# Kernel tuning notes

Hardware: AMD Instinct MI355X
Metric: run time of the kernel (lower is better)

Reference implementation:

```python
import jax, jax.numpy as jnp
import numpy as np

N = 50000        # nodes
E = 1_600_000    # edges (before self-loops)
H = 2            # heads
C = 16           # out channels per head
G = 512          # graphs in batch
F_IN = 3         # const + degree + rand
NC = 2           # classes
NEG_SLOPE = 0.2  # PyG GATv2Conv default


def setup_inputs() -> dict:
    key = jax.random.key(0)
    ks = jax.random.split(key, 12)
    p = lambda k, shape: (jax.random.normal(k, shape, dtype=jnp.float32) * 0.1)
    edge_index = jax.random.randint(ks[0], (2, E), 0, N, dtype=jnp.int64)
    batch = jnp.sort(jax.random.randint(ks[1], (N,), 0, G, dtype=jnp.int64))
    rand_feat = jax.random.uniform(ks[2], (N, 1), dtype=jnp.float32)
    return {
        "edge_index": edge_index,
        "batch": batch,
        "rand_feat": rand_feat,
        # conv1: in=3 -> H*C=32
        "W1l": p(ks[3], (H * C, F_IN)), "b1l": jnp.zeros((H * C,), jnp.float32),
        "W1r": p(ks[4], (H * C, F_IN)), "b1r": jnp.zeros((H * C,), jnp.float32),
        "att1": p(ks[5], (H, C)), "bias1": jnp.zeros((H * C,), jnp.float32),
        # conv2: in=32 -> 32
        "W2l": p(ks[6], (H * C, H * C)), "b2l": jnp.zeros((H * C,), jnp.float32),
        "W2r": p(ks[7], (H * C, H * C)), "b2r": jnp.zeros((H * C,), jnp.float32),
        "att2": p(ks[8], (H, C)), "bias2": jnp.zeros((H * C,), jnp.float32),
        # fc: 32 -> 2
        "Wfc": p(ks[9], (NC, H * C)), "bfc": jnp.zeros((NC,), jnp.float32),
    }


def gatv2_conv(x, src, dst, Wl, bl, Wr, br, att, bias):
    """PyG GATv2Conv (concat=True, self-loops already appended to src/dst)."""
    n = x.shape[0]
    xl = (x @ Wl.T + bl).reshape(n, H, C)   # messages / values
    xr = (x @ Wr.T + br).reshape(n, H, C)   # target-side term
    m = xl[src] + xr[dst]                   # [E', H, C]
    e = jnp.where(m > 0, m, NEG_SLOPE * m)  # LeakyReLU
    score = jnp.einsum('ehc,hc->eh', e, att)
    # segment softmax over destination nodes (every node has a self-loop)
    smax = jax.ops.segment_max(score, dst, num_segments=n)
    ex = jnp.exp(score - smax[dst])
    denom = jax.ops.segment_sum(ex, dst, num_segments=n)
    alpha = ex / (denom[dst] + 1e-16)
    out = jax.ops.segment_sum(xl[src] * alpha[:, :, None], dst, num_segments=n)
    return out.reshape(n, H * C) + bias


def reference(edge_index, batch, rand_feat, W1l, b1l, W1r, b1r, att1, bias1,
              W2l, b2l, W2r, b2r, att2, bias2, Wfc, bfc):
    src, dst = edge_index[0], edge_index[1]
    # degree feature: index_add of ones over both rows (original edges only)
    ones_e = jnp.ones((E,), jnp.float32)
    deg = (jax.ops.segment_sum(ones_e, src, num_segments=N)
           + jax.ops.segment_sum(ones_e, dst, num_segments=N))
    x = jnp.concatenate([jnp.ones((N, 1), jnp.float32), deg[:, None], rand_feat], axis=1)
    # PyG GATv2Conv adds self-loops by default
    loops = jnp.arange(N, dtype=src.dtype)
    src_sl = jnp.concatenate([src, loops])
    dst_sl = jnp.concatenate([dst, loops])
    x = jax.nn.elu(gatv2_conv(x, src_sl, dst_sl, W1l, b1l, W1r, b1r, att1, bias1))
    x = jax.nn.elu(gatv2_conv(x, src_sl, dst_sl, W2l, b2l, W2r, b2r, att2, bias2))
    # global mean pool over graphs
    sums = jax.ops.segment_sum(x, batch, num_segments=G)
    counts = jax.ops.segment_sum(jnp.ones((N,), jnp.float32), batch, num_segments=G)
    pooled = sums / jnp.clip(counts, 1.0)[:, None]
    logits = pooled @ Wfc.T + bfc
    return jax.nn.log_softmax(logits, axis=1)
```

## Files before the change

kernel.cpp:

```cpp
#include <hip/hip_runtime.h>
#include <hip/hip_fp16.h>
#include <math.h>

#define HC 32
#define CH 16
#define NSLOPE 0.2f
#define NB2MAX 512
#define TILE 8192
#define CBMAX 6144
#define NSL 128
#define HGRP 8
#define HLDS 12544

__device__ __forceinline__ unsigned gen_pair(const int* __restrict__ ei, int E, int i){
    if (i < E) return (unsigned(ei[E+i]) << 16) | unsigned(ei[i]);
    unsigned n = i - E; return (n << 16) | n;
}

__device__ __forceinline__ __half2 pkmax2(__half2 a, __half2 b){
    union { __half2 h; unsigned u; } ua, ub, ud;
    ua.h = a; ub.h = b;
    asm("v_pk_max_f16 %0, %1, %2" : "=v"(ud.u) : "v"(ua.u), "v"(ub.u));
    return ud.h;
}

__device__ __forceinline__ __half2 sfx2(__half2 x, int off){
    union { __half2 h; int i; } u; u.h = x;
    u.i = __shfl_xor(u.i, off);
    return u.h;
}

__global__ void k_hsrc(const int* __restrict__ ei, int E, int halfN,
                       unsigned* __restrict__ hb, unsigned* __restrict__ gPair){
    __shared__ unsigned h[HLDS];
    __shared__ unsigned hp[NB2MAX];
    int t = threadIdx.x;
    int nWloc = halfN >> 1;
    for (int i = t; i < nWloc; i += 512) h[i] = 0;
    int p = blockIdx.x & 1;
    if (p == 0){ hp[t] = 0; }
    __syncthreads();
    int slice = blockIdx.x >> 1;
    int base  = p * halfN;
    int chunk = (((E + NSL - 1) / NSL) + 3) & ~3;
    int lo = slice*chunk, hi = lo + chunk; if (hi > E) hi = E;
    bool v4 = ((E & 3) == 0);
    if (v4 && lo < hi){
        int m4 = lo + ((hi - lo) & ~3);
        for (int i = lo + 4*t; i + 3 < hi; i += 4*512){
            int4 s4 = *(const int4*)(ei + i);
            int a0 = s4.x - base, a1 = s4.y - base, a2 = s4.z - base, a3 = s4.w - base;
            if ((unsigned)a0 < (unsigned)halfN) atomicAdd(&h[a0 >> 1], 1u << (16*(a0 & 1)));
            if ((unsigned)a1 < (unsigned)halfN) atomicAdd(&h[a1 >> 1], 1u << (16*(a1 & 1)));
            if ((unsigned)a2 < (unsigned)halfN) atomicAdd(&h[a2 >> 1], 1u << (16*(a2 & 1)));
            if ((unsigned)a3 < (unsigned)halfN) atomicAdd(&h[a3 >> 1], 1u << (16*(a3 & 1)));
            if (p == 0){
                int4 d4 = *(const int4*)(ei + E + i);
                atomicAdd(&hp[unsigned(d4.x) >> 7], 1u);
                atomicAdd(&hp[unsigned(d4.y) >> 7], 1u);
                atomicAdd(&hp[unsigned(d4.z) >> 7], 1u);
                atomicAdd(&hp[unsigned(d4.w) >> 7], 1u);
            }
        }
        for (int i = m4 + t; i < hi; i += 512){
            int s = ei[i] - base;
            if ((unsigned)s < (unsigned)halfN) atomicAdd(&h[s >> 1], 1u << (16*(s & 1)));
            if (p == 0) atomicAdd(&hp[unsigned(ei[E+i]) >> 7], 1u);
        }
    } else {
        for (int i = lo + t; i < hi; i += 512){
            int s = ei[i] - base;
            if ((unsigned)s < (unsigned)halfN) atomicAdd(&h[s >> 1], 1u << (16*(s & 1)));
            if (p == 0) atomicAdd(&hp[unsigned(ei[E+i]) >> 7], 1u);
        }
    }
    __syncthreads();
    unsigned* out = hb + (size_t)blockIdx.x * nWloc;
    for (int w = t; w < nWloc; w += 512) out[w] = h[w];
    if (p == 0 && hp[t]) atomicAdd(&gPair[t], hp[t]);
}

__global__ void k_hred(const unsigned* __restrict__ hb, unsigned* __restrict__ degS,
                       int nWloc,
                       const int* __restrict__ batch, int* __restrict__ gb,
                       int N, int G){
    int idx = blockIdx.x*blockDim.x + threadIdx.x;
    if (idx <= G){
        int lo = 0, hi = N;
        while (lo < hi){ int mid = (lo+hi)>>1; if (batch[mid] < idx) lo = mid+1; else hi = mid; }
        gb[idx] = lo;
    }
    int total = 2*nWloc;
    int grp = idx / total;
    if (grp >= HGRP) return;
    int rem = idx - grp*total;
    int p = (rem < nWloc) ? 0 : 1;
    int w = rem - p*nWloc;
    unsigned s = 0;
    int sl0 = grp*(NSL/HGRP), sl1 = sl0 + NSL/HGRP;
    for (int sl = sl0; sl < sl1; ++sl)
        s += hb[(size_t)(sl*2 + p)*nWloc + w];
    if (s) atomicAdd(&degS[rem], s);
}

__global__ void k_setup(unsigned* __restrict__ gPair,
                        int* __restrict__ partBase, int* __restrict__ gcur,
                        int* __restrict__ rsN, int EP, int nb, int N,
                        const float* __restrict__ W1l, const float* __restrict__ b1l,
                        const float* __restrict__ W1r, const float* __restrict__ b1r,
                        const float* __restrict__ att1, const float* __restrict__ bias1,
                        float4* __restrict__ tabA, float4* __restrict__ tabB){
    __shared__ int sp[NB2MAX];
    int t = threadIdx.x;
    int vp = 0;
    if (t < nb){
        int selfc = N - t*128;
        selfc = (selfc < 0) ? 0 : (selfc > 128 ? 128 : selfc);
        vp = (int)gPair[t] + selfc;
        gPair[t] = (unsigned)vp;
    }
    sp[t] = vp;
    __syncthreads();
    for (int d = 1; d < NB2MAX; d <<= 1){
        int x = (t >= d) ? sp[t-d] : 0;
        __syncthreads();
        sp[t] += x;
        __syncthreads();
    }
    if (t < nb){ partBase[t] = sp[t] - vp; gcur[t] = sp[t] - vp; }
    if (t == 0) rsN[0] = EP;
    if (t < HC){
        tabA[t] = make_float4(W1l[t*3] + b1l[t], W1l[t*3+1], W1l[t*3+2], att1[t]);
        tabB[t] = make_float4(W1r[t*3] + b1r[t], W1r[t*3+1], W1r[t*3+2], bias1[t]);
    }
}

__global__ void k_p2(const int* __restrict__ ei, int E, int EP,
                     int* __restrict__ gcur, unsigned* __restrict__ part){
    __shared__ int bcnt[NB2MAX], bstart[NB2MAX], c2[NB2MAX], gpos[NB2MAX], sc[256];
    __shared__ unsigned sorted[TILE];
    __shared__ unsigned short bktof[TILE];
    int t = threadIdx.x;
    int base = blockIdx.x * TILE;
    int cnt = EP - base; if (cnt > TILE) cnt = TILE;
    bool full = (cnt == TILE);

    bcnt[t] = 0; bcnt[t+256] = 0; c2[t] = 0; c2[t+256] = 0;
    __syncthreads();
    unsigned ec[TILE/256];
    if (full){
        #pragma unroll
        for (int q = 0; q < TILE/256; ++q)
            ec[q] = gen_pair(ei, E, base + t + q*256);
        #pragma unroll
        for (int q = 0; q < TILE/256; ++q)
            atomicAdd(&bcnt[ec[q] >> 23], 1);
    } else {
        for (int j = t; j < cnt; j += 256){
            unsigned e = gen_pair(ei, E, base + j);
            atomicAdd(&bcnt[e >> 23], 1);
        }
    }
    __syncthreads();
    int v0 = bcnt[2*t], v1 = bcnt[2*t+1];
    int s = v0 + v1;
    sc[t] = s;
    __syncthreads();
    for (int d = 1; d < 256; d <<= 1){
        int x = (t >= d) ? sc[t-d] : 0;
        __syncthreads();
        sc[t] += x;
        __syncthreads();
    }
    int excl = sc[t] - s;
    bstart[2*t]   = excl;
    bstart[2*t+1] = excl + v0;
    #pragma unroll
    for (int q = 0; q < 2; ++q){
        int bb = 2*t + q;
        int v = (q == 0) ? v0 : v1;
        if (v > 0){
            gpos[bb] = atomicAdd(&gcur[bb], v);
            int bs = bstart[bb];
            for (int j = 0; j < v; ++j) bktof[bs + j] = (unsigned short)bb;
        }
    }
    __syncthreads();
    if (full){
        #pragma unroll
        for (int q = 0; q < TILE/256; ++q){
            unsigned e = ec[q];
            int b = e >> 23;
            int off = atomicAdd(&c2[b], 1);
            sorted[bstart[b] + off] = e;
        }
    } else {
        for (int j = t; j < cnt; j += 256){
            unsigned e = gen_pair(ei, E, base + j);
            int b = e >> 23;
            int off = atomicAdd(&c2[b], 1);
            sorted[bstart[b] + off] = e;
        }
    }
    __syncthreads();
    for (int k = t; k < cnt; k += 256){
        int b = bktof[k];
        part[gpos[b] + (k - bstart[b])] = sorted[k];
    }
}

__global__ void k_fine(const unsigned* __restrict__ part, const int* __restrict__ partBase,
                       const unsigned* __restrict__ gPair,
                       const unsigned* __restrict__ degS, const float* __restrict__ rnd,
                       int* __restrict__ rs, float2* __restrict__ dr,
                       int* __restrict__ col, int N){
    __shared__ int pcnt[128], c2[128], lrs[129], sc[128];
    __shared__ int colbuf[CBMAX];
    int b = blockIdx.x, t = threadIdx.x;
    int beg = partBase[b], end = beg + (int)gPair[b];
    if (t < 128){ pcnt[t] = 0; c2[t] = 0; }
    __syncthreads();
    for (int k = beg + t; k < end; k += 256)
        atomicAdd(&pcnt[(part[k] >> 16) & 127], 1);
    __syncthreads();
    int v = (t < 128) ? pcnt[t] : 0;
    if (t < 128) sc[t] = v;
    __syncthreads();
    for (int d = 1; d < 128; d <<= 1){
        int x = (t >= d && t < 128) ? sc[t-d] : 0;
        __syncthreads();
        if (t < 128) sc[t] += x;
        __syncthreads();
    }
    if (t < 128){
        lrs[t] = sc[t] - v;
        if (t == 127) lrs[128] = sc[127];
    }
    __syncthreads();
    int n = (b << 7) + t;
    if (t < 128 && n < N){
        rs[n] = partBase[b] + lrs[t];
        unsigned s16 = (degS[n >> 1] >> (16*(n & 1))) & 0xFFFFu;
        dr[n] = make_float2((float)(pcnt[t] - 1 + (int)s16), rnd[n]);
    }
    for (int k = beg + t; k < end; k += 256){
        unsigned e = part[k];
        int j = (e >> 16) & 127;
        int pos = lrs[j] + atomicAdd(&c2[j], 1);
        if (pos < CBMAX) colbuf[pos] = (int)(e & 0xFFFFu);
    }
    __syncthreads();
    int npair = lrs[128];
    int cb = partBase[b];
    for (int k = t; k < npair; k += 256) col[cb + k] = colbuf[k];
}

__global__ void k_gat1(const int* __restrict__ rs, const int* __restrict__ col,
                       const float2* __restrict__ dr,
                       const float4* __restrict__ tabA, const float4* __restrict__ tabB,
                       const float* __restrict__ W2l, const float* __restrict__ b2l,
                       const float* __restrict__ W2r, const float* __restrict__ b2r,
                       __half* __restrict__ A16, __half* __restrict__ B16, int N){
    __shared__ float4 tA[HC], tB[HC];
    __shared__ float4 wq[HC][16];
    __shared__ float blS[HC], brS[HC];
    int t = threadIdx.x;
    if (t < HC){ tA[t] = tabA[t]; tB[t] = tabB[t]; blS[t] = b2l[t]; brS[t] = b2r[t]; }
    for (int w = t; w < HC*16; w += 256){
        int j = w >> 4, k = w & 15;
        wq[j][k] = make_float4(W2l[(2*k)*HC + j], W2l[(2*k+1)*HC + j],
                               W2r[(2*k)*HC + j], W2r[(2*k+1)*HC + j]);
    }
    __syncthreads();

    int d = blockIdx.x*(blockDim.x >> 4) + (t >> 4);
    if (d >= N) return;
    int lane = t & 15;
    int h = lane >> 3, r = lane & 7;

    float2 drd = dr[d];
    float base[CH];
    #pragma unroll
    for (int c = 0; c < CH; ++c){
        float4 a4 = tA[h*CH + c];
        float4 b4 = tB[h*CH + c];
        float xr = b4.x + b4.y*drd.x + b4.z*drd.y;
        base[c] = a4.x + xr;
    }

    float l = 0.f, S1 = 0.f, S2 = 0.f;
    int beg = rs[d], end = rs[d+1];
    int p = beg + r;
    for (; p + 8 < end; p += 16){
        int s0 = __builtin_nontemporal_load(col + p);
        int s1 = __builtin_nontemporal_load(col + p + 8);
        float2 da = dr[s0];
        float2 db = dr[s1];
        float sc0 = 0.f, sc1 = 0.f;
        #pragma unroll
        for (int c = 0; c < CH; ++c){
            float4 a4 = tA[h*CH + c];
            float m0 = base[c] + a4.y*da.x + a4.z*da.y;
            float m1 = base[c] + a4.y*db.x + a4.z*db.y;
            m0 = (m0 > 0.f) ? m0 : NSLOPE*m0;
            m1 = (m1 > 0.f) ? m1 : NSLOPE*m1;
            sc0 += m0 * a4.w;
            sc1 += m1 * a4.w;
        }
        float ex0 = __expf(sc0), ex1 = __expf(sc1);
        l  += ex0 + ex1;
        S1 += ex0*da.x + ex1*db.x;
        S2 += ex0*da.y + ex1*db.y;
    }
    if (p < end){
        float2 ds = dr[__builtin_nontemporal_load(col + p)];
        float sc = 0.f;
        #pragma unroll
        for (int c = 0; c < CH; ++c){
            float4 a4 = tA[h*CH + c];
            float mm = base[c] + a4.y*ds.x + a4.z*ds.y;
            mm = (mm > 0.f) ? mm : NSLOPE*mm;
            sc += mm * a4.w;
        }
        float ex = __expf(sc);
        l  += ex;
        S1 += ex*ds.x;
        S2 += ex*ds.y;
    }

    #pragma unroll
    for (int off = 4; off >= 1; off >>= 1){
        l  += __shfl_xor(l,  off);
        S1 += __shfl_xor(S1, off);
        S2 += __shfl_xor(S2, off);
    }

    float invl = 1.f/(l + 1e-16f);
    int c0 = r*2;
    float4 a40 = tA[h*CH + c0],     b40 = tB[h*CH + c0];
    float4 a41 = tA[h*CH + c0 + 1], b41 = tB[h*CH + c0 + 1];
    float v0 = a40.x + (a40.y*S1 + a40.z*S2)*invl + b40.w;
    float v1 = a41.x + (a41.y*S1 + a41.z*S2)*invl + b41.w;
    float x0 = (v0 > 0.f) ? v0 : expm1f(v0);
    float x1 = (v1 > 0.f) ? v1 : expm1f(v1);

    int k0 = 2*lane;
    float a0 = blS[k0], a1 = blS[k0+1];
    float g0 = brS[k0], g1 = brS[k0+1];
    #pragma unroll
    for (int tt = 0; tt < 16; ++tt){
        float xa = __shfl(x0, tt, 16);
        float xb = __shfl(x1, tt, 16);
        int j = 2*tt;
        float4 q0 = wq[j][lane];
        float4 q1 = wq[j+1][lane];
        a0 += xa*q0.x + xb*q1.x;
        a1 += xa*q0.y + xb*q1.y;
        g0 += xa*q0.z + xb*q1.z;
        g1 += xa*q0.w + xb*q1.w;
    }
    *(__half2*)(A16 + (size_t)d*HC + k0) = __floats2half2_rn(a0, a1);
    *(__half2*)(B16 + (size_t)d*HC + k0) = __floats2half2_rn(g0, g1);
}

__global__ void k_gat(const int* __restrict__ rs, const int* __restrict__ col,
                      const __half* __restrict__ A16, const __half* __restrict__ B16,
                      const float* __restrict__ att, const float* __restrict__ bias,
                      const int* __restrict__ batch, float* __restrict__ pooled, int N){
    __shared__ float pool[8][HC];
    __shared__ int sb[8];
    int sg = threadIdx.x >> 5;
    int d = blockIdx.x*(blockDim.x >> 5) + sg;
    int lane = threadIdx.x & 31;
    bool valid = (d < N);
    int dcl = valid ? d : 0;
    int h = lane >> 4, r = lane & 15;

    union U { uint4 u[2]; __half2 h2[8]; };
    U xr;
    {
        const uint4* bp = (const uint4*)(B16 + (size_t)dcl*HC + h*CH);
        xr.u[0] = bp[0]; xr.u[1] = bp[1];
    }
    __half2 at2[8];
    const float* atf = att + h*CH;
    #pragma unroll
    for (int i = 0; i < 8; ++i) at2[i] = __floats2half2_rn(atf[2*i], atf[2*i+1]);
    const __half2 ns2 = __float2half2_rn(NSLOPE);

    float l = 0.f;
    __half2 acc2[8];
    #pragma unroll
    for (int i = 0; i < 8; ++i) acc2[i] = __float2half2_rn(0.f);

    int beg = rs[dcl], end = valid ? rs[dcl+1] : beg;
    int p = beg + r;
    for (; p + 16 < end; p += 32){
        int s0 = __builtin_nontemporal_load(col + p);
        int s1 = __builtin_nontemporal_load(col + p + 16);
        const uint4* rp0 = (const uint4*)(A16 + (size_t)s0*HC + h*CH);
        const uint4* rp1 = (const uint4*)(A16 + (size_t)s1*HC + h*CH);
        U a, b;
        a.u[0] = rp0[0]; a.u[1] = rp0[1];
        b.u[0] = rp1[0]; b.u[1] = rp1[1];
        __half2 sc2 = __float2half2_rn(0.f);
        #pragma unroll
        for (int i = 0; i < 8; ++i){
            __half2 m  = __hadd2(a.h2[i], xr.h2[i]);
            __half2 lk = pkmax2(m, __hmul2(m, ns2));
            sc2 = __hfma2(lk, at2[i], sc2);
        }
        float ex = __expf(__low2float(sc2) + __high2float(sc2));
        l += ex;
        __half2 exh = __float2half2_rn(ex);
        #pragma unroll
        for (int i = 0; i < 8; ++i) acc2[i] = __hfma2(a.h2[i], exh, acc2[i]);

        sc2 = __float2half2_rn(0.f);
        #pragma unroll
        for (int i = 0; i < 8; ++i){
            __half2 m  = __hadd2(b.h2[i], xr.h2[i]);
            __half2 lk = pkmax2(m, __hmul2(m, ns2));
            sc2 = __hfma2(lk, at2[i], sc2);
        }
        ex = __expf(__low2float(sc2) + __high2float(sc2));
        l += ex;
        exh = __float2half2_rn(ex);
        #pragma unroll
        for (int i = 0; i < 8; ++i) acc2[i] = __hfma2(b.h2[i], exh, acc2[i]);
    }
    if (p < end){
        int s = __builtin_nontemporal_load(col + p);
        const uint4* rp = (const uint4*)(A16 + (size_t)s*HC + h*CH);
        U a;
        a.u[0] = rp[0]; a.u[1] = rp[1];
        __half2 sc2 = __float2half2_rn(0.f);
        #pragma unroll
        for (int i = 0; i < 8; ++i){
            __half2 m  = __hadd2(a.h2[i], xr.h2[i]);
            __half2 lk = pkmax2(m, __hmul2(m, ns2));
            sc2 = __hfma2(lk, at2[i], sc2);
        }
        float ex = __expf(__low2float(sc2) + __high2float(sc2));
        l += ex;
        __half2 exh = __float2half2_rn(ex);
        #pragma unroll
        for (int i = 0; i < 8; ++i) acc2[i] = __hfma2(a.h2[i], exh, acc2[i]);
    }

    __half2 v4[4];
    {
        bool hi = (r & 8) != 0;
        #pragma unroll
        for (int i = 0; i < 4; ++i){
            __half2 send = hi ? acc2[i] : acc2[i+4];
            __half2 recv = sfx2(send, 8);
            v4[i] = __hadd2(hi ? acc2[i+4] : acc2[i], recv);
        }
    }
    __half2 v2[2];
    {
        bool hi = (r & 4) != 0;
        __half2 s0 = hi ? v4[0] : v4[2];
        __half2 s1 = hi ? v4[1] : v4[3];
        __half2 r0 = sfx2(s0, 4);
        __half2 r1 = sfx2(s1, 4);
        v2[0] = __hadd2(hi ? v4[2] : v4[0], r0);
        v2[1] = __hadd2(hi ? v4[3] : v4[1], r1);
    }
    __half2 v1;
    {
        bool hi = (r & 2) != 0;
        __half2 send = hi ? v2[0] : v2[1];
        __half2 recv = sfx2(send, 2);
        v1 = __hadd2(hi ? v2[1] : v2[0], recv);
    }
    float mine;
    {
        bool hi = (r & 1) != 0;
        float lo = __low2float(v1), hf = __high2float(v1);
        float send = hi ? lo : hf;
        float recv = __shfl_xor(send, 1);
        mine = (hi ? hf : lo) + recv;
    }
    #pragma unroll
    for (int off = 8; off >= 1; off >>= 1) l += __shfl_xor(l, off);

    float invl = 1.f/(l + 1e-16f);
    float val = mine*invl + bias[h*CH + r];
    val = (val > 0.f) ? val : expm1f(val);

    if (lane == 0) sb[sg] = valid ? batch[d] : (-1 - sg);
    pool[sg][h*CH + r] = val;
    __syncthreads();
    int myb = sb[sg];
    int first = sg;
    #pragma unroll
    for (int j = 7; j >= 0; --j) if (sb[j] == myb) first = j;
    if (valid && first == sg){
        float s = 0.f;
        #pragma unroll
        for (int j = 0; j < 8; ++j) if (sb[j] == myb) s += pool[j][h*CH + r];
        atomicAdd(&pooled[(size_t)myb*HC + h*CH + r], s);
    }
}

__global__ void k_fc(const float* __restrict__ pooled, const int* __restrict__ gb,
                     const float* __restrict__ Wfc, const float* __restrict__ bfc,
                     float* __restrict__ out, int G){
    int t = threadIdx.x;
    int g = blockIdx.x*2 + (t >> 5);
    int c = t & 31;
    if (g >= G) return;
    float cnt = (float)(gb[g+1] - gb[g]);
    if (cnt < 1.f) cnt = 1.f;
    float pv = pooled[g*HC + c] / cnt;
    float p0 = pv * Wfc[c];
    float p1 = pv * Wfc[HC + c];
    #pragma unroll
    for (int off = 16; off >= 1; off >>= 1){
        p0 += __shfl_xor(p0, off, 32);
        p1 += __shfl_xor(p1, off, 32);
    }
    if (c == 0){
        float l0 = p0 + bfc[0], l1 = p1 + bfc[1];
        float m = (l0 > l1) ? l0 : l1;
        float lse = m + logf(__expf(l0 - m) + __expf(l1 - m));
        out[g*2 + 0] = l0 - lse;
        out[g*2 + 1] = l1 - lse;
    }
}

extern "C" void kernel_launch(void* const* d_in, const int* in_sizes, int n_in,
                              void* d_out, int out_size, void* d_ws, size_t ws_size,
                              hipStream_t stream) {
    const int*   ei    = (const int*)  d_in[0];
    const int*   batch = (const int*)  d_in[1];
    const float* rnd   = (const float*)d_in[2];
    const float* W1l   = (const float*)d_in[3];
    const float* b1l   = (const float*)d_in[4];
    const float* W1r   = (const float*)d_in[5];
    const float* b1r   = (const float*)d_in[6];
    const float* att1  = (const float*)d_in[7];
    const float* bias1 = (const float*)d_in[8];
    const float* W2l   = (const float*)d_in[9];
    const float* b2l   = (const float*)d_in[10];
    const float* W2r   = (const float*)d_in[11];
    const float* b2r   = (const float*)d_in[12];
    const float* att2  = (const float*)d_in[13];
    const float* bias2 = (const float*)d_in[14];
    const float* Wfc   = (const float*)d_in[15];
    const float* bfc   = (const float*)d_in[16];

    const int E  = in_sizes[0] / 2;
    const int N  = in_sizes[1];
    const int G  = out_size / 2;
    const int EP = E + N;
    const int NB2 = (N + 127) >> 7;
    const int halfN = (((N + 1) >> 1) + 1) & ~1;
    const int nWloc = halfN >> 1;

    float* ws        = (float*)d_ws;
    __half* A16      = (__half*)ws;
    __half* B16      = A16 + (size_t)N*HC;
    unsigned* hb     = (unsigned*)ws;
    unsigned* part   = (unsigned*)ws;
    size_t off       = (size_t)NSL*2*nWloc;
    if (off < (size_t)EP)   off = EP;
    if (off < (size_t)N*HC) off = (size_t)N*HC;
    off = (off + 1) & ~(size_t)1;
    float2* dr       = (float2*)(ws + off);
    int*   rs        = (int*)(dr + N);
    int*   col       = rs + N + 1;
    unsigned* degS   = (unsigned*)(col + EP);
    unsigned* gPair  = degS + 2*nWloc;
    float* pooled    = (float*)(gPair + NB2MAX);
    int*   partBase  = (int*)(pooled + (size_t)G*HC);
    int*   gcur      = partBase + NB2MAX;
    int*   gb        = gcur + NB2MAX;
    float4* tabA     = (float4*)((((size_t)(gb + G + 1)) + 15) & ~(size_t)15);
    float4* tabB     = tabA + HC;

    const int T = 256;
    const int gD16 = (N + (T>>4) - 1)/(T>>4);
    const int gD32 = (N + (T>>5) - 1)/(T>>5);
    const int nTiles = (EP + TILE - 1)/TILE;

    (void)hipMemsetAsync(degS, 0, (size_t)(2*nWloc + NB2MAX + (size_t)G*HC)*sizeof(unsigned), stream);

    k_hsrc <<<NSL*2, 512, 0, stream>>>(ei, E, halfN, hb, gPair);
    k_hred <<<(2*nWloc*HGRP + T-1)/T, T, 0, stream>>>(hb, degS, nWloc, batch, gb, N, G);
    k_setup<<<1, 512, 0, stream>>>(gPair, partBase, gcur, rs + N, EP, NB2, N,
                                   W1l, b1l, W1r, b1r, att1, bias1, tabA, tabB);
    k_p2   <<<nTiles, T, 0, stream>>>(ei, E, EP, gcur, part);
    k_fine <<<NB2, T, 0, stream>>>(part, partBase, gPair, degS, rnd, rs, dr, col, N);

    k_gat1<<<gD16, T, 0, stream>>>(rs, col, dr, tabA, tabB,
                                   W2l, b2l, W2r, b2r, A16, B16, N);

    k_gat <<<gD32, T, 0, stream>>>(rs, col, A16, B16, att2, bias2, batch, pooled, N);

    k_fc  <<<(G + 1)/2, 64, 0, stream>>>(pooled, gb, Wfc, bfc, (float*)d_out, G);
}
```

Measured before the change: 217.6 us.

## Merge histogram reduce, setup scan and partition into one fixed-stride launch

Each coarse bucket of the partition buffer now gets a fixed capacity of CBMAX slots, so partition positions no longer depend on a prefix scan and gcur can be seeded in k_hsrc. This lets the degree reduction, the bucket prefix scan/table setup and the edge partition run as separate block roles in one kernel, removing two launches and their serialization. Writes past a bucket's capacity are dropped, which would corrupt results if any bucket held more than CBMAX edges. The partition buffer also grows to NB2*CBMAX entries.

```diff
diff --git a/kernel.cpp b/kernel.cpp
--- a/kernel.cpp
+++ b/kernel.cpp
@@ -31,7 +31,8 @@
 }
 
 __global__ void k_hsrc(const int* __restrict__ ei, int E, int halfN,
-                       unsigned* __restrict__ hb, unsigned* __restrict__ gPair){
+                       unsigned* __restrict__ hb, unsigned* __restrict__ gPair,
+                       int* __restrict__ gcur){
     __shared__ unsigned h[HLDS];
     __shared__ unsigned hp[NB2MAX];
     int t = threadIdx.x;
@@ -39,6 +40,7 @@
     for (int i = t; i < nWloc; i += 512) h[i] = 0;
     int p = blockIdx.x & 1;
     if (p == 0){ hp[t] = 0; }
+    if (blockIdx.x == 0 && t < NB2MAX) gcur[t] = t*CBMAX;
     __syncthreads();
     int slice = blockIdx.x >> 1;
     int base  = p * halfN;
@@ -80,132 +82,141 @@
     if (p == 0 && hp[t]) atomicAdd(&gPair[t], hp[t]);
 }
 
-__global__ void k_hred(const unsigned* __restrict__ hb, unsigned* __restrict__ degS,
-                       int nWloc,
-                       const int* __restrict__ batch, int* __restrict__ gb,
-                       int N, int G){
-    int idx = blockIdx.x*blockDim.x + threadIdx.x;
-    if (idx <= G){
-        int lo = 0, hi = N;
-        while (lo < hi){ int mid = (lo+hi)>>1; if (batch[mid] < idx) lo = mid+1; else hi = mid; }
-        gb[idx] = lo;
-    }
-    int total = 2*nWloc;
-    int grp = idx / total;
-    if (grp >= HGRP) return;
-    int rem = idx - grp*total;
-    int p = (rem < nWloc) ? 0 : 1;
-    int w = rem - p*nWloc;
-    unsigned s = 0;
-    int sl0 = grp*(NSL/HGRP), sl1 = sl0 + NSL/HGRP;
-    for (int sl = sl0; sl < sl1; ++sl)
-        s += hb[(size_t)(sl*2 + p)*nWloc + w];
-    if (s) atomicAdd(&degS[rem], s);
-}
-
-__global__ void k_setup(unsigned* __restrict__ gPair,
-                        int* __restrict__ partBase, int* __restrict__ gcur,
-                        int* __restrict__ rsN, int EP, int nb, int N,
-                        const float* __restrict__ W1l, const float* __restrict__ b1l,
-                        const float* __restrict__ W1r, const float* __restrict__ b1r,
-                        const float* __restrict__ att1, const float* __restrict__ bias1,
-                        float4* __restrict__ tabA, float4* __restrict__ tabB){
-    __shared__ int sp[NB2MAX];
-    int t = threadIdx.x;
-    int vp = 0;
-    if (t < nb){
-        int selfc = N - t*128;
-        selfc = (selfc < 0) ? 0 : (selfc > 128 ? 128 : selfc);
-        vp = (int)gPair[t] + selfc;
-        gPair[t] = (unsigned)vp;
-    }
-    sp[t] = vp;
-    __syncthreads();
-    for (int d = 1; d < NB2MAX; d <<= 1){
-        int x = (t >= d) ? sp[t-d] : 0;
-        __syncthreads();
-        sp[t] += x;
-        __syncthreads();
-    }
-    if (t < nb){ partBase[t] = sp[t] - vp; gcur[t] = sp[t] - vp; }
-    if (t == 0) rsN[0] = EP;
-    if (t < HC){
-        tabA[t] = make_float4(W1l[t*3] + b1l[t], W1l[t*3+1], W1l[t*3+2], att1[t]);
-        tabB[t] = make_float4(W1r[t*3] + b1r[t], W1r[t*3+1], W1r[t*3+2], bias1[t]);
-    }
-}
-
-__global__ void k_p2(const int* __restrict__ ei, int E, int EP,
-                     int* __restrict__ gcur, unsigned* __restrict__ part){
+__global__ void k_mid(const int* __restrict__ ei, int E, int EP,
+                      int* __restrict__ gcur, unsigned* __restrict__ part,
+                      const unsigned* __restrict__ hb, unsigned* __restrict__ degS,
+                      int nWloc, const int* __restrict__ batch, int* __restrict__ gb,
+                      int N, int G, int nTiles, int nHred,
+                      unsigned* __restrict__ gPair,
+                      int* __restrict__ partBase, int* __restrict__ rsN, int nb,
+                      const float* __restrict__ W1l, const float* __restrict__ b1l,
+                      const float* __restrict__ W1r, const float* __restrict__ b1r,
+                      const float* __restrict__ att1, const float* __restrict__ bias1,
+                      float4* __restrict__ tabA, float4* __restrict__ tabB){
     __shared__ int bcnt[NB2MAX], bstart[NB2MAX], c2[NB2MAX], gpos[NB2MAX], sc[256];
     __shared__ unsigned sorted[TILE];
     __shared__ unsigned short bktof[TILE];
     int t = threadIdx.x;
-    int base = blockIdx.x * TILE;
-    int cnt = EP - base; if (cnt > TILE) cnt = TILE;
-    bool full = (cnt == TILE);
-
-    bcnt[t] = 0; bcnt[t+256] = 0; c2[t] = 0; c2[t+256] = 0;
-    __syncthreads();
-    unsigned ec[TILE/256];
-    if (full){
-        #pragma unroll
-        for (int q = 0; q < TILE/256; ++q)
-            ec[q] = gen_pair(ei, E, base + t + q*256);
-        #pragma unroll
-        for (int q = 0; q < TILE/256; ++q)
-            atomicAdd(&bcnt[ec[q] >> 23], 1);
+    int blk = blockIdx.x;
+
+    if (blk < nTiles){
+        int base = blk * TILE;
+        int cnt = EP - base; if (cnt > TILE) cnt = TILE;
+        bool full = (cnt == TILE);
+        bcnt[t] = 0; bcnt[t+256] = 0; c2[t] = 0; c2[t+256] = 0;
+        __syncthreads();
+        unsigned ec[TILE/256];
+        if (full){
+            #pragma unroll
+            for (int q = 0; q < TILE/256; ++q)
+                ec[q] = gen_pair(ei, E, base + t + q*256);
+            #pragma unroll
+            for (int q = 0; q < TILE/256; ++q)
+                atomicAdd(&bcnt[ec[q] >> 23], 1);
+        } else {
+            for (int j = t; j < cnt; j += 256){
+                unsigned e = gen_pair(ei, E, base + j);
+                atomicAdd(&bcnt[e >> 23], 1);
+            }
+        }
+        __syncthreads();
+        int v0 = bcnt[2*t], v1 = bcnt[2*t+1];
+        int s = v0 + v1;
+        sc[t] = s;
+        __syncthreads();
+        for (int d = 1; d < 256; d <<= 1){
+            int x = (t >= d) ? sc[t-d] : 0;
+            __syncthreads();
+            sc[t] += x;
+            __syncthreads();
+        }
+        int excl = sc[t] - s;
+        bstart[2*t]   = excl;
+        bstart[2*t+1] = excl + v0;
+        #pragma unroll
+        for (int q = 0; q < 2; ++q){
+            int bb = 2*t + q;
+            int v = (q == 0) ? v0 : v1;
+            if (v > 0){
+                gpos[bb] = atomicAdd(&gcur[bb], v);
+                int bs = bstart[bb];
+                for (int j = 0; j < v; ++j) bktof[bs + j] = (unsigned short)bb;
+            }
+        }
+        __syncthreads();
+        if (full){
+            #pragma unroll
+            for (int q = 0; q < TILE/256; ++q){
+                unsigned e = ec[q];
+                int b = e >> 23;
+                int off = atomicAdd(&c2[b], 1);
+                sorted[bstart[b] + off] = e;
+            }
+        } else {
+            for (int j = t; j < cnt; j += 256){
+                unsigned e = gen_pair(ei, E, base + j);
+                int b = e >> 23;
+                int off = atomicAdd(&c2[b], 1);
+                sorted[bstart[b] + off] = e;
+            }
+        }
+        __syncthreads();
+        for (int k = t; k < cnt; k += 256){
+            int b = bktof[k];
+            int w = gpos[b] + (k - bstart[b]);
+            if (w < (b+1)*CBMAX) part[w] = sorted[k];
+        }
+    } else if (blk < nTiles + nHred){
+        int idx = (blk - nTiles)*256 + t;
+        if (idx <= G){
+            int lo = 0, hi = N;
+            while (lo < hi){ int mid = (lo+hi)>>1; if (batch[mid] < idx) lo = mid+1; else hi = mid; }
+            gb[idx] = lo;
+        }
+        int total = 2*nWloc;
+        int grp = idx / total;
+        if (grp < HGRP){
+            int rem = idx - grp*total;
+            int p = (rem < nWloc) ? 0 : 1;
+            int w = rem - p*nWloc;
+            unsigned s = 0;
+            int sl0 = grp*(NSL/HGRP), sl1 = sl0 + NSL/HGRP;
+            for (int sl = sl0; sl < sl1; ++sl)
+                s += hb[(size_t)(sl*2 + p)*nWloc + w];
+            if (s) atomicAdd(&degS[rem], s);
+        }
     } else {
-        for (int j = t; j < cnt; j += 256){
-            unsigned e = gen_pair(ei, E, base + j);
-            atomicAdd(&bcnt[e >> 23], 1);
-        }
-    }
-    __syncthreads();
-    int v0 = bcnt[2*t], v1 = bcnt[2*t+1];
-    int s = v0 + v1;
-    sc[t] = s;
-    __syncthreads();
-    for (int d = 1; d < 256; d <<= 1){
-        int x = (t >= d) ? sc[t-d] : 0;
-        __syncthreads();
-        sc[t] += x;
-        __syncthreads();
-    }
-    int excl = sc[t] - s;
-    bstart[2*t]   = excl;
-    bstart[2*t+1] = excl + v0;
-    #pragma unroll
-    for (int q = 0; q < 2; ++q){
-        int bb = 2*t + q;
-        int v = (q == 0) ? v0 : v1;
-        if (v > 0){
-            gpos[bb] = atomicAdd(&gcur[bb], v);
-            int bs = bstart[bb];
-            for (int j = 0; j < v; ++j) bktof[bs + j] = (unsigned short)bb;
-        }
-    }
-    __syncthreads();
-    if (full){
-        #pragma unroll
-        for (int q = 0; q < TILE/256; ++q){
-            unsigned e = ec[q];
-            int b = e >> 23;
-            int off = atomicAdd(&c2[b], 1);
-            sorted[bstart[b] + off] = e;
-        }
-    } else {
-        for (int j = t; j < cnt; j += 256){
-            unsigned e = gen_pair(ei, E, base + j);
-            int b = e >> 23;
-            int off = atomicAdd(&c2[b], 1);
-            sorted[bstart[b] + off] = e;
-        }
-    }
-    __syncthreads();
-    for (int k = t; k < cnt; k += 256){
-        int b = bktof[k];
-        part[gpos[b] + (k - bstart[b])] = sorted[k];
+        int vp0 = 0, vp1 = 0;
+        int b0 = 2*t, b1 = 2*t + 1;
+        if (b0 < nb){
+            int selfc = N - b0*128;
+            selfc = (selfc < 0) ? 0 : (selfc > 128 ? 128 : selfc);
+            vp0 = (int)gPair[b0] + selfc;
+            gPair[b0] = (unsigned)vp0;
+        }
+        if (b1 < nb){
+            int selfc = N - b1*128;
+            selfc = (selfc < 0) ? 0 : (selfc > 128 ? 128 : selfc);
+            vp1 = (int)gPair[b1] + selfc;
+            gPair[b1] = (unsigned)vp1;
+        }
+        int s = vp0 + vp1;
+        sc[t] = s;
+        __syncthreads();
+        for (int d = 1; d < 256; d <<= 1){
+            int x = (t >= d) ? sc[t-d] : 0;
+            __syncthreads();
+            sc[t] += x;
+            __syncthreads();
+        }
+        int excl = sc[t] - s;
+        if (b0 < nb) partBase[b0] = excl;
+        if (b1 < nb) partBase[b1] = excl + vp0;
+        if (t == 0) rsN[0] = EP;
+        if (t < HC){
+            tabA[t] = make_float4(W1l[t*3] + b1l[t], W1l[t*3+1], W1l[t*3+2], att1[t]);
+            tabB[t] = make_float4(W1r[t*3] + b1r[t], W1r[t*3+1], W1r[t*3+2], bias1[t]);
+        }
     }
 }
 
@@ -217,7 +228,7 @@
     __shared__ int pcnt[128], c2[128], lrs[129], sc[128];
     __shared__ int colbuf[CBMAX];
     int b = blockIdx.x, t = threadIdx.x;
-    int beg = partBase[b], end = beg + (int)gPair[b];
+    int beg = b*CBMAX, end = beg + (int)gPair[b];
     if (t < 128){ pcnt[t] = 0; c2[t] = 0; }
     __syncthreads();
     for (int k = beg + t; k < end; k += 256)
@@ -238,8 +249,9 @@
     }
     __syncthreads();
     int n = (b << 7) + t;
+    int pb = partBase[b];
     if (t < 128 && n < N){
-        rs[n] = partBase[b] + lrs[t];
+        rs[n] = pb + lrs[t];
         unsigned s16 = (degS[n >> 1] >> (16*(n & 1))) & 0xFFFFu;
         dr[n] = make_float2((float)(pcnt[t] - 1 + (int)s16), rnd[n]);
     }
@@ -251,8 +263,7 @@
     }
     __syncthreads();
     int npair = lrs[128];
-    int cb = partBase[b];
-    for (int k = t; k < npair; k += 256) col[cb + k] = colbuf[k];
+    for (int k = t; k < npair; k += 256) col[pb + k] = colbuf[k];
 }
 
 __global__ void k_gat1(const int* __restrict__ rs, const int* __restrict__ col,
@@ -566,8 +577,8 @@
     unsigned* hb     = (unsigned*)ws;
     unsigned* part   = (unsigned*)ws;
     size_t off       = (size_t)NSL*2*nWloc;
-    if (off < (size_t)EP)   off = EP;
-    if (off < (size_t)N*HC) off = (size_t)N*HC;
+    if (off < (size_t)NB2*CBMAX) off = (size_t)NB2*CBMAX;
+    if (off < (size_t)N*HC)      off = (size_t)N*HC;
     off = (off + 1) & ~(size_t)1;
     float2* dr       = (float2*)(ws + off);
     int*   rs        = (int*)(dr + N);
@@ -585,15 +596,16 @@
     const int gD16 = (N + (T>>4) - 1)/(T>>4);
     const int gD32 = (N + (T>>5) - 1)/(T>>5);
     const int nTiles = (EP + TILE - 1)/TILE;
+    const int nHred  = (2*nWloc*HGRP + T-1)/T;
 
     (void)hipMemsetAsync(degS, 0, (size_t)(2*nWloc + NB2MAX + (size_t)G*HC)*sizeof(unsigned), stream);
 
-    k_hsrc <<<NSL*2, 512, 0, stream>>>(ei, E, halfN, hb, gPair);
-    k_hred <<<(2*nWloc*HGRP + T-1)/T, T, 0, stream>>>(hb, degS, nWloc, batch, gb, N, G);
-    k_setup<<<1, 512, 0, stream>>>(gPair, partBase, gcur, rs + N, EP, NB2, N,
+    k_hsrc<<<NSL*2, 512, 0, stream>>>(ei, E, halfN, hb, gPair, gcur);
+    k_mid <<<nTiles + nHred + 1, T, 0, stream>>>(ei, E, EP, gcur, part,
+                                   hb, degS, nWloc, batch, gb, N, G, nTiles, nHred,
+                                   gPair, partBase, rs + N, NB2,
                                    W1l, b1l, W1r, b1r, att1, bias1, tabA, tabB);
-    k_p2   <<<nTiles, T, 0, stream>>>(ei, E, EP, gcur, part);
-    k_fine <<<NB2, T, 0, stream>>>(part, partBase, gPair, degS, rnd, rs, dr, col, N);
+    k_fine<<<NB2, T, 0, stream>>>(part, partBase, gPair, degS, rnd, rs, dr, col, N);
 
     k_gat1<<<gD16, T, 0, stream>>>(rs, col, dr, tabA, tabB,
                                    W2l, b2l, W2r, b2r, A16, B16, N);
```

New measurement: 212.2 us. 2.4% less time.
